# Optimization experiments

Hardware: AMD Instinct MI355X
Metric: run time of the kernel (lower is better)

## Reference

```python
import jax, jax.numpy as jnp
import numpy as np

B, L, HID, H = 2, 384, 512, 8
D = HID // H  # head_dim = 64


def setup_inputs() -> dict:
    key = jax.random.key(0)
    ks = jax.random.split(key, 16)
    s = 0.02
    return {
        "query": jax.random.normal(ks[0], (B, L, HID), jnp.float32),
        "key_": jax.random.normal(ks[1], (B, L, HID), jnp.float32),
        "value": jax.random.normal(ks[2], (B, L, HID), jnp.float32),
        "mask": jnp.ones((B, 1, 1, L), jnp.int32),
        # fc_q/k/v/o: nn.Linear(hid_dim, hid_dim)
        "Wq": jax.random.normal(ks[3], (HID, HID), jnp.float32) * s,
        "bq": jnp.zeros((HID,), jnp.float32),
        "Wk": jax.random.normal(ks[4], (HID, HID), jnp.float32) * s,
        "bk": jnp.zeros((HID,), jnp.float32),
        "Wv": jax.random.normal(ks[5], (HID, HID), jnp.float32) * s,
        "bv": jnp.zeros((HID,), jnp.float32),
        "Wo": jax.random.normal(ks[6], (HID, HID), jnp.float32) * s,
        "bo": jnp.zeros((HID,), jnp.float32),
        # additive-attention score MLP: W1, W2: Linear(D, D); v: Linear(D, 1)
        "W1": jax.random.normal(ks[7], (D, D), jnp.float32) * s,
        "b1": jnp.zeros((D,), jnp.float32),
        "W2": jax.random.normal(ks[8], (D, D), jnp.float32) * s,
        "b2": jnp.zeros((D,), jnp.float32),
        "vw": jax.random.normal(ks[9], (1, D), jnp.float32) * s,
        "vb": jnp.zeros((1,), jnp.float32),
    }


def reference(query, key_, value, mask, Wq, bq, Wk, bk, Wv, bv, Wo, bo,
              W1, b1, W2, b2, vw, vb):
    b = query.shape[0]
    # projections (torch Linear: x @ W.T + b)
    Q = query @ Wq.T + bq
    K = key_ @ Wk.T + bk
    V = value @ Wv.T + bv
    # [b, h, l, d]
    def split_heads(x):
        return x.reshape(b, -1, H, D).transpose(0, 2, 1, 3)
    Q, K, V = split_heads(Q), split_heads(K), split_heads(V)
    # additive (Bahdanau-style) score: v^T tanh(W1 q + W2 k)
    tQ = Q @ W1.T + b1            # [b, h, lq, d]
    tK = K @ W2.T + b2            # [b, h, lk, d]
    e = jnp.tanh(tQ[:, :, :, None, :] + tK[:, :, None, :, :])  # [b,h,lq,lk,d]
    energy = jnp.einsum('bhqkd,d->bhqk', e, vw[0]) + vb[0]      # [b,h,lq,lk]
    energy = jnp.where(mask == 0, jnp.float32(-1e10), energy)
    attention = jax.nn.softmax(energy, axis=-1)
    x = jnp.einsum('bhqk,bhkd->bhqd', attention, V)  # dropout p=0 (eval)
    x = x.transpose(0, 2, 1, 3).reshape(b, -1, HID)
    x = x @ Wo.T + bo
    return x, attention
```

## Files before the change

### kernel.cpp

```cpp
#include <hip/hip_runtime.h>

#define BATCH 2
#define LSEQ 384
#define NHID 512
#define NH 8
#define DH 64
#define BH (BATCH*NH)
#define MROWS (BATCH*LSEQ)
#define XELEMS ((size_t)MROWS * NHID)
#define TQ 4
#define QTILES (LSEQ/TQ)

typedef unsigned short ushort_t;

__device__ __forceinline__ float bf2f(ushort_t u) {
    unsigned int v = ((unsigned int)u) << 16;
    return __uint_as_float(v);
}
__device__ __forceinline__ ushort_t f2bf(float f) {
    unsigned int u = __float_as_uint(f);
    unsigned int lsb = (u >> 16) & 1u;
    u += 0x7fffu + lsb;
    return (ushort_t)(u >> 16);
}
__device__ __forceinline__ float ld1(const void* p, size_t i, int f) {
    return f ? ((const float*)p)[i] : bf2f(((const ushort_t*)p)[i]);
}
__device__ __forceinline__ float4 ld4(const void* p, size_t i, int f) {
    if (f) return ((const float4*)p)[i >> 2];
    ushort4 u = ((const ushort4*)p)[i >> 2];
    return make_float4(bf2f(u.x), bf2f(u.y), bf2f(u.z), bf2f(u.w));
}
__device__ __forceinline__ int block_detect(const unsigned int* q, int* cnt) {
    int t = threadIdx.x;
    if (t == 0) *cnt = 0;
    __syncthreads();
    int n = blockDim.x < 256 ? blockDim.x : 256;
    if (t < n) {
        unsigned int elo = (q[t] >> 7) & 0xFFu;
        if (elo >= 100u && elo <= 150u) atomicAdd(cnt, 1);
    }
    __syncthreads();
    return (*cnt * 2 > n) ? 0 : 1;
}

#define OFF_P     16
#define PSTRIDE   393216
#define OFF_BQE   2359312
#define OFF_BKE   2359824
#define OFF_ETQ   2360336
#define OFF_ETKT  2753552
#define OFF_VH    3146768
#define OFF_XH    3539984

#define MICRO_FMA(a, b)                                                  \
    acc[0][0] = fmaf(a.x, b.x, acc[0][0]); acc[0][1] = fmaf(a.x, b.y, acc[0][1]); \
    acc[0][2] = fmaf(a.x, b.z, acc[0][2]); acc[0][3] = fmaf(a.x, b.w, acc[0][3]); \
    acc[1][0] = fmaf(a.y, b.x, acc[1][0]); acc[1][1] = fmaf(a.y, b.y, acc[1][1]); \
    acc[1][2] = fmaf(a.y, b.z, acc[1][2]); acc[1][3] = fmaf(a.y, b.w, acc[1][3]); \
    acc[2][0] = fmaf(a.z, b.x, acc[2][0]); acc[2][1] = fmaf(a.z, b.y, acc[2][1]); \
    acc[2][2] = fmaf(a.z, b.z, acc[2][2]); acc[2][3] = fmaf(a.z, b.w, acc[2][3]); \
    acc[3][0] = fmaf(a.w, b.x, acc[3][0]); acc[3][1] = fmaf(a.w, b.y, acc[3][1]); \
    acc[3][2] = fmaf(a.w, b.z, acc[3][2]); acc[3][3] = fmaf(a.w, b.w, acc[3][3])

#define FMA4(dst, p, v)  dst.x = fmaf(p, v.x, dst.x); dst.y = fmaf(p, v.y, dst.y); \
                         dst.z = fmaf(p, v.z, dst.z); dst.w = fmaf(p, v.w, dst.w)

__global__ __launch_bounds__(128) void gemm_qkv(
    const void* qp, const void* kp, const void* vp,
    const void* Wqp, const void* Wkp, const void* Wvp,
    const void* W1p, const void* W2p,
    const void* bqp, const void* bkp, const void* b1p, const void* b2p,
    float* __restrict__ ws)
{
    __shared__ int s_cnt;
    __shared__ __align__(16) float smem[6656];
    const int f = block_detect((const unsigned int*)qp, &s_cnt);

    const int z = blockIdx.z;
    const int mode = z >> 1, ks = z & 1;
    const int kbase = ks * 256;
    const void* A = (mode == 0) ? qp : (mode == 1) ? kp : vp;
    const void* W = (mode == 0) ? Wqp : (mode == 1) ? Wkp : Wvp;
    float* P = ws + OFF_P + (size_t)z * PSTRIDE;

    float* As = smem;
    float* Bs = smem + 1152;

    const int row0 = blockIdx.y * 32;
    const int col0 = blockIdx.x * 64;
    const int tid = threadIdx.x;

    const int alr = tid >> 2, alc = tid & 3;
    const int blr = tid >> 1, blc = tid & 1;
    const int tm = tid >> 4, tn = tid & 15;

    const size_t abase = (size_t)(row0 + alr) * 512;
    const size_t bbase = (size_t)(col0 + blr) * 512;

    float4 a0, a1, b0, b1, b2, b3;
    a0 = ld4(A, abase + kbase + alc * 4, f);
    a1 = ld4(A, abase + kbase + (alc + 4) * 4, f);
    b0 = ld4(W, bbase + kbase + (blc + 0) * 4, f);
    b1 = ld4(W, bbase + kbase + (blc + 2) * 4, f);
    b2 = ld4(W, bbase + kbase + (blc + 4) * 4, f);
    b3 = ld4(W, bbase + kbase + (blc + 6) * 4, f);

    float acc[4][4];
    #pragma unroll
    for (int i = 0; i < 4; i++)
        #pragma unroll
        for (int j = 0; j < 4; j++) acc[i][j] = 0.f;

    for (int k0 = kbase; k0 < kbase + 256; k0 += 32) {
        __syncthreads();
        As[(alc * 4 + 0) * 36 + alr] = a0.x; As[(alc * 4 + 1) * 36 + alr] = a0.y;
        As[(alc * 4 + 2) * 36 + alr] = a0.z; As[(alc * 4 + 3) * 36 + alr] = a0.w;
        As[((alc + 4) * 4 + 0) * 36 + alr] = a1.x; As[((alc + 4) * 4 + 1) * 36 + alr] = a1.y;
        As[((alc + 4) * 4 + 2) * 36 + alr] = a1.z; As[((alc + 4) * 4 + 3) * 36 + alr] = a1.w;
        Bs[((blc + 0) * 4 + 0) * 68 + blr] = b0.x; Bs[((blc + 0) * 4 + 1) * 68 + blr] = b0.y;
        Bs[((blc + 0) * 4 + 2) * 68 + blr] = b0.z; Bs[((blc + 0) * 4 + 3) * 68 + blr] = b0.w;
        Bs[((blc + 2) * 4 + 0) * 68 + blr] = b1.x; Bs[((blc + 2) * 4 + 1) * 68 + blr] = b1.y;
        Bs[((blc + 2) * 4 + 2) * 68 + blr] = b1.z; Bs[((blc + 2) * 4 + 3) * 68 + blr] = b1.w;
        Bs[((blc + 4) * 4 + 0) * 68 + blr] = b2.x; Bs[((blc + 4) * 4 + 1) * 68 + blr] = b2.y;
        Bs[((blc + 4) * 4 + 2) * 68 + blr] = b2.z; Bs[((blc + 4) * 4 + 3) * 68 + blr] = b2.w;
        Bs[((blc + 6) * 4 + 0) * 68 + blr] = b3.x; Bs[((blc + 6) * 4 + 1) * 68 + blr] = b3.y;
        Bs[((blc + 6) * 4 + 2) * 68 + blr] = b3.z; Bs[((blc + 6) * 4 + 3) * 68 + blr] = b3.w;
        __syncthreads();
        int k1 = k0 + 32;
        if (k1 < kbase + 256) {
            a0 = ld4(A, abase + k1 + alc * 4, f);
            a1 = ld4(A, abase + k1 + (alc + 4) * 4, f);
            b0 = ld4(W, bbase + k1 + (blc + 0) * 4, f);
            b1 = ld4(W, bbase + k1 + (blc + 2) * 4, f);
            b2 = ld4(W, bbase + k1 + (blc + 4) * 4, f);
            b3 = ld4(W, bbase + k1 + (blc + 6) * 4, f);
        }
        #pragma unroll
        for (int kk = 0; kk < 32; kk++) {
            float4 a = *reinterpret_cast<const float4*>(&As[kk * 36 + tm * 4]);
            float4 b = *reinterpret_cast<const float4*>(&Bs[kk * 68 + tn * 4]);
            MICRO_FMA(a, b);
        }
    }

    if (mode == 2) {
        #pragma unroll
        for (int i = 0; i < 4; i++) {
            int m = row0 + tm * 4 + i;
            float4 o4 = make_float4(acc[i][0], acc[i][1], acc[i][2], acc[i][3]);
            *reinterpret_cast<float4*>(&P[(size_t)m * 512 + col0 + tn * 4]) = o4;
        }
    } else {
        const void* W1x = mode ? W2p : W1p;
        float* Qs  = smem;
        float* W1s = smem + 2304;
        __syncthreads();
        #pragma unroll
        for (int i = 0; i < 4; i++)
            #pragma unroll
            for (int j = 0; j < 4; j++)
                Qs[(tn * 4 + j) * 36 + tm * 4 + i] = acc[i][j];
        {
            int od = tid >> 1;
            #pragma unroll
            for (int c = 0; c < 8; c++) {
                int j = (tid & 1) * 32 + c * 4;
                float4 w = ld4(W1x, (size_t)od * 64 + j, f);
                W1s[(j + 0) * 68 + od] = w.x; W1s[(j + 1) * 68 + od] = w.y;
                W1s[(j + 2) * 68 + od] = w.z; W1s[(j + 3) * 68 + od] = w.w;
            }
        }
        __syncthreads();
        float facc[4][4];
        #pragma unroll
        for (int i = 0; i < 4; i++)
            #pragma unroll
            for (int j = 0; j < 4; j++) facc[i][j] = 0.f;
        {
            float acc[4][4];
            #pragma unroll
            for (int i = 0; i < 4; i++)
                #pragma unroll
                for (int j = 0; j < 4; j++) acc[i][j] = 0.f;
            #pragma unroll 8
            for (int kk = 0; kk < 64; kk++) {
                float4 a = *reinterpret_cast<const float4*>(&Qs[kk * 36 + tm * 4]);
                float4 b = *reinterpret_cast<const float4*>(&W1s[kk * 68 + tn * 4]);
                MICRO_FMA(a, b);
            }
            #pragma unroll
            for (int i = 0; i < 4; i++)
                #pragma unroll
                for (int j = 0; j < 4; j++) facc[i][j] = acc[i][j];
        }
        #pragma unroll
        for (int i = 0; i < 4; i++) {
            int m = row0 + tm * 4 + i;
            float4 o4 = make_float4(facc[i][0], facc[i][1], facc[i][2], facc[i][3]);
            *reinterpret_cast<float4*>(&P[(size_t)m * 512 + col0 + tn * 4]) = o4;
        }
        if (blockIdx.y == 0 && ks == 0 && tid < 64) {
            int o = col0 + tid, od = o & 63, h = o >> 6;
            const void* b1x = mode ? b2p : b1p;
            const void* bx  = mode ? bkp : bqp;
            float s = ld1(b1x, od, f);
            for (int j = 0; j < 64; j++)
                s = fmaf(ld1(W1x, (size_t)od * 64 + j, f), ld1(bx, h * 64 + j, f), s);
            ws[(mode ? OFF_BKE : OFF_BQE) + o] = s;
        }
    }
}

__global__ __launch_bounds__(256) void finalize(
    const void* qp, const void* bvp,
    const float* __restrict__ ws_in, float* __restrict__ ws)
{
    __shared__ int s_cnt;
    __shared__ __align__(16) float T[64 * 68];
    const int f = block_detect((const unsigned int*)qp, &s_cnt);
    const int blk = blockIdx.x;
    const int tid = threadIdx.x;

    if (blk < 384 || blk >= 480) {
        const int isV = (blk >= 480);
        const float* P0 = ws_in + OFF_P + (size_t)(isV ? 4 : 0) * PSTRIDE;
        const float* P1 = P0 + PSTRIDE;
        float* Out = ws + (isV ? OFF_VH : OFF_ETQ);
        int gid = (isV ? blk - 480 : blk) * 256 + tid;
        int m = gid >> 7;
        int o4 = (gid & 127) * 4;
        float4 p0 = *reinterpret_cast<const float4*>(P0 + (size_t)m * 512 + o4);
        float4 p1 = *reinterpret_cast<const float4*>(P1 + (size_t)m * 512 + o4);
        float4 bb;
        if (isV) bb = ld4(bvp, o4, f);
        else     bb = *reinterpret_cast<const float4*>(ws_in + OFF_BQE + o4);
        float4 r;
        if (isV) {
            r.x = p0.x + p1.x + bb.x; r.y = p0.y + p1.y + bb.y;
            r.z = p0.z + p1.z + bb.z; r.w = p0.w + p1.w + bb.w;
        } else {
            r.x = __expf(2.f * (p0.x + p1.x + bb.x));
            r.y = __expf(2.f * (p0.y + p1.y + bb.y));
            r.z = __expf(2.f * (p0.z + p1.z + bb.z));
            r.w = __expf(2.f * (p0.w + p1.w + bb.w));
        }
        int b = m / LSEQ, l = m % LSEQ, h = o4 >> 6, d = o4 & 63;
        *reinterpret_cast<float4*>(&Out[(size_t)((b * NH + h) * LSEQ + l) * 64 + d]) = r;
    } else {
        int blk2 = blk - 384;
        int bh = blk2 / 6, l0 = (blk2 % 6) * 64;
        int b = bh >> 3, h = bh & 7;
        const float* P0 = ws_in + OFF_P + (size_t)2 * PSTRIDE;
        const float* P1 = P0 + PSTRIDE;
        #pragma unroll
        for (int it = 0; it < 4; it++) {
            int li = (tid >> 4) + it * 16;
            int d4 = (tid & 15) * 4;
            size_t src = (size_t)(b * LSEQ + l0 + li) * 512 + h * 64 + d4;
            float4 p0 = *reinterpret_cast<const float4*>(P0 + src);
            float4 p1 = *reinterpret_cast<const float4*>(P1 + src);
            const float4 bb = *reinterpret_cast<const float4*>(ws_in + OFF_BKE + h * 64 + d4);
            T[(d4 + 0) * 68 + li] = __expf(2.f * (p0.x + p1.x + bb.x));
            T[(d4 + 1) * 68 + li] = __expf(2.f * (p0.y + p1.y + bb.y));
            T[(d4 + 2) * 68 + li] = __expf(2.f * (p0.z + p1.z + bb.z));
            T[(d4 + 3) * 68 + li] = __expf(2.f * (p0.w + p1.w + bb.w));
        }
        __syncthreads();
        float* Out = ws + OFF_ETKT;
        #pragma unroll
        for (int it = 0; it < 4; it++) {
            int d = (tid >> 4) + it * 16;
            int l4 = (tid & 15) * 4;
            float4 v = *reinterpret_cast<const float4*>(&T[d * 68 + l4]);
            *reinterpret_cast<float4*>(&Out[(size_t)(bh * 64 + d) * LSEQ + l0 + l4]) = v;
        }
    }
}

__global__ __launch_bounds__(384, 6) void attn_kernel(
    const void* qp, const void* vwp, const void* vbp,
    const float* __restrict__ ws_in, float* __restrict__ ws,
    const int* __restrict__ mask, void* __restrict__ dout)
{
    __shared__ int s_cnt;
    const int f = block_detect((const unsigned int*)qp, &s_cnt);

    const float* Etq = ws_in + OFF_ETQ;
    const float* Etk = ws_in + OFF_ETKT;
    const float* Vh  = ws_in + OFF_VH;
    float* Xh = ws + OFF_XH;

    const int bid = blockIdx.x;
    const int qt = bid % QTILES;
    const int bh = bid / QTILES;
    const int q0 = qt * TQ;
    const int b  = bh >> 3;
    const int h  = bh & 7;
    const int t  = threadIdx.x;
    const int wave = t >> 6;

    __shared__ __align__(16) float etqT[64][TQ];
    __shared__ float iws[64];
    __shared__ float ps[TQ][LSEQ];
    __shared__ float red[6][TQ][16][4];
    __shared__ float rmax[TQ][6];
    __shared__ float rsum[TQ][6];
    __shared__ float s_vb;

    if (t < 256) {
        int d = t & 63, qi = t >> 6;
        float vwv = ld1(vwp, d, f);
        float iw = __builtin_amdgcn_rcpf(vwv);
        etqT[d][qi] = Etq[(size_t)(bh * LSEQ + q0 + qi) * 64 + d] * iw;
        if (qi == 0) {
            iws[d] = iw;
            float v = vwv;
            #pragma unroll
            for (int off = 32; off > 0; off >>= 1) v += __shfl_xor(v, off, 64);
            if (d == 0) s_vb = ld1(vbp, 0, f) + v;
        }
    }
    const int mok = mask[b * LSEQ + t];
    __syncthreads();
    const float vbSum = s_vb;

    float e2[TQ] = {0.f, 0.f, 0.f, 0.f};
    const float* ekp = Etk + (size_t)bh * 64 * LSEQ + t;
    #pragma unroll 4
    for (int d = 0; d < 64; d++) {
        float ekv = ekp[(size_t)d * LSEQ];
        float4 eq = *reinterpret_cast<const float4*>(&etqT[d][0]);
        float iw = iws[d];
        e2[0] += __builtin_amdgcn_rcpf(fmaf(eq.x, ekv, iw));
        e2[1] += __builtin_amdgcn_rcpf(fmaf(eq.y, ekv, iw));
        e2[2] += __builtin_amdgcn_rcpf(fmaf(eq.z, ekv, iw));
        e2[3] += __builtin_amdgcn_rcpf(fmaf(eq.w, ekv, iw));
    }
    float en[TQ];
    #pragma unroll
    for (int qi = 0; qi < TQ; qi++) {
        en[qi] = fmaf(-2.0f, e2[qi], vbSum);
        if (mok == 0) en[qi] = -1e10f;
    }

    #pragma unroll
    for (int qi = 0; qi < TQ; qi++) {
        float m = en[qi];
        #pragma unroll
        for (int off = 32; off > 0; off >>= 1) m = fmaxf(m, __shfl_xor(m, off, 64));
        if ((t & 63) == 0) rmax[qi][wave] = m;
    }
    __syncthreads();
    float p[TQ];
    #pragma unroll
    for (int qi = 0; qi < TQ; qi++) {
        float gm = fmaxf(fmaxf(fmaxf(rmax[qi][0], rmax[qi][1]),
                               fmaxf(rmax[qi][2], rmax[qi][3])),
                         fmaxf(rmax[qi][4], rmax[qi][5]));
        p[qi] = __expf(en[qi] - gm);
        float s = p[qi];
        #pragma unroll
        for (int off = 32; off > 0; off >>= 1) s += __shfl_xor(s, off, 64);
        if ((t & 63) == 0) rsum[qi][wave] = s;
    }
    __syncthreads();
    #pragma unroll
    for (int qi = 0; qi < TQ; qi++) {
        float gs = rsum[qi][0] + rsum[qi][1] + rsum[qi][2] +
                   rsum[qi][3] + rsum[qi][4] + rsum[qi][5];
        p[qi] *= 1.0f / gs;
        ps[qi][t] = p[qi];
        size_t aidx = XELEMS + (size_t)(bh * LSEQ + q0 + qi) * LSEQ + t;
        if (f) ((float*)dout)[aidx] = p[qi];
        else   ((ushort_t*)dout)[aidx] = f2bf(p[qi]);
    }
    __syncthreads();

    const int dq = t & 15;
    const int ksub = t >> 4;
    const float* vb4 = Vh + (size_t)bh * LSEQ * 64 + dq * 4;
    float4 acc[TQ];
    #pragma unroll
    for (int qi = 0; qi < TQ; qi++) acc[qi] = make_float4(0.f, 0.f, 0.f, 0.f);
    for (int kk = ksub; kk < LSEQ; kk += 24) {
        float4 v4 = *reinterpret_cast<const float4*>(vb4 + (size_t)kk * 64);
        #pragma unroll
        for (int qi = 0; qi < TQ; qi++) {
            float pq = ps[qi][kk];
            FMA4(acc[qi], pq, v4);
        }
    }
    #pragma unroll
    for (int qi = 0; qi < TQ; qi++) {
        #pragma unroll
        for (int off = 16; off <= 32; off <<= 1) {
            acc[qi].x += __shfl_xor(acc[qi].x, off, 64);
            acc[qi].y += __shfl_xor(acc[qi].y, off, 64);
            acc[qi].z += __shfl_xor(acc[qi].z, off, 64);
            acc[qi].w += __shfl_xor(acc[qi].w, off, 64);
        }
    }
    if ((t & 63) < 16) {
        #pragma unroll
        for (int qi = 0; qi < TQ; qi++) {
            red[wave][qi][dq][0] = acc[qi].x;
            red[wave][qi][dq][1] = acc[qi].y;
            red[wave][qi][dq][2] = acc[qi].z;
            red[wave][qi][dq][3] = acc[qi].w;
        }
    }
    __syncthreads();
    if (t < 256) {
        int qi = t >> 6, d = t & 63;
        float sx = 0.f;
        #pragma unroll
        for (int w = 0; w < 6; w++) sx += red[w][qi][d >> 2][d & 3];
        Xh[((size_t)(b * LSEQ + q0 + qi) * NH + h) * 64 + d] = sx;
    }
}

__global__ __launch_bounds__(128) void gemm_out(
    const void* qp, const void* Wop, const void* bop,
    const float* __restrict__ ws_in, void* __restrict__ dout)
{
    __shared__ int s_cnt;
    __shared__ __align__(16) float As[32][36];
    __shared__ __align__(16) float Bs[32][68];
    const int f = block_detect((const unsigned int*)qp, &s_cnt);

    const float* Xh = ws_in + OFF_XH;
    const int row0 = blockIdx.y * 32;
    const int col0 = blockIdx.x * 64;
    const int tid = threadIdx.x;

    const int alr = tid >> 2, alc = tid & 3;
    const int blr = tid >> 1, blc = tid & 1;
    const int tm = tid >> 4, tn = tid & 15;

    const float* Ab = Xh + (size_t)(row0 + alr) * 512;
    const size_t bbase = (size_t)(col0 + blr) * 512;

    float4 a0, a1, b0, b1, b2, b3;
    a0 = *reinterpret_cast<const float4*>(Ab + alc * 4);
    a1 = *reinterpret_cast<const float4*>(Ab + (alc + 4) * 4);
    b0 = ld4(Wop, bbase + (blc + 0) * 4, f);
    b1 = ld4(Wop, bbase + (blc + 2) * 4, f);
    b2 = ld4(Wop, bbase + (blc + 4) * 4, f);
    b3 = ld4(Wop, bbase + (blc + 6) * 4, f);

    float acc[4][4];
    #pragma unroll
    for (int i = 0; i < 4; i++)
        #pragma unroll
        for (int j = 0; j < 4; j++) acc[i][j] = 0.f;

    for (int k0 = 0; k0 < 512; k0 += 32) {
        __syncthreads();
        As[alc * 4 + 0][alr] = a0.x; As[alc * 4 + 1][alr] = a0.y;
        As[alc * 4 + 2][alr] = a0.z; As[alc * 4 + 3][alr] = a0.w;
        As[(alc + 4) * 4 + 0][alr] = a1.x; As[(alc + 4) * 4 + 1][alr] = a1.y;
        As[(alc + 4) * 4 + 2][alr] = a1.z; As[(alc + 4) * 4 + 3][alr] = a1.w;
        Bs[(blc + 0) * 4 + 0][blr] = b0.x; Bs[(blc + 0) * 4 + 1][blr] = b0.y;
        Bs[(blc + 0) * 4 + 2][blr] = b0.z; Bs[(blc + 0) * 4 + 3][blr] = b0.w;
        Bs[(blc + 2) * 4 + 0][blr] = b1.x; Bs[(blc + 2) * 4 + 1][blr] = b1.y;
        Bs[(blc + 2) * 4 + 2][blr] = b1.z; Bs[(blc + 2) * 4 + 3][blr] = b1.w;
        Bs[(blc + 4) * 4 + 0][blr] = b2.x; Bs[(blc + 4) * 4 + 1][blr] = b2.y;
        Bs[(blc + 4) * 4 + 2][blr] = b2.z; Bs[(blc + 4) * 4 + 3][blr] = b2.w;
        Bs[(blc + 6) * 4 + 0][blr] = b3.x; Bs[(blc + 6) * 4 + 1][blr] = b3.y;
        Bs[(blc + 6) * 4 + 2][blr] = b3.z; Bs[(blc + 6) * 4 + 3][blr] = b3.w;
        __syncthreads();
        int k1 = k0 + 32;
        if (k1 < 512) {
            a0 = *reinterpret_cast<const float4*>(Ab + k1 + alc * 4);
            a1 = *reinterpret_cast<const float4*>(Ab + k1 + (alc + 4) * 4);
            b0 = ld4(Wop, bbase + k1 + (blc + 0) * 4, f);
            b1 = ld4(Wop, bbase + k1 + (blc + 2) * 4, f);
            b2 = ld4(Wop, bbase + k1 + (blc + 4) * 4, f);
            b3 = ld4(Wop, bbase + k1 + (blc + 6) * 4, f);
        }
        #pragma unroll
        for (int kk = 0; kk < 32; kk++) {
            float4 a = *reinterpret_cast<const float4*>(&As[kk][tm * 4]);
            float4 b = *reinterpret_cast<const float4*>(&Bs[kk][tn * 4]);
            MICRO_FMA(a, b);
        }
    }

    #pragma unroll
    for (int i = 0; i < 4; i++) {
        int m = row0 + tm * 4 + i;
        #pragma unroll
        for (int j = 0; j < 4; j++) {
            int n = col0 + tn * 4 + j;
            float c = acc[i][j] + ld1(bop, n, f);
            size_t idx = (size_t)m * 512 + n;
            if (f) ((float*)dout)[idx] = c;
            else   ((ushort_t*)dout)[idx] = f2bf(c);
        }
    }
}

extern "C" void kernel_launch(void* const* d_in, const int* in_sizes, int n_in,
                              void* d_out, int out_size, void* d_ws, size_t ws_size,
                              hipStream_t stream)
{
    const void* qp = d_in[0];
    const void* kp = d_in[1];
    const void* vp = d_in[2];
    const int* mask = (const int*)d_in[3];
    const void* Wqp = d_in[4];  const void* bqp = d_in[5];
    const void* Wkp = d_in[6];  const void* bkp = d_in[7];
    const void* Wvp = d_in[8];  const void* bvp = d_in[9];
    const void* Wop = d_in[10]; const void* bop = d_in[11];
    const void* W1p = d_in[12]; const void* b1p = d_in[13];
    const void* W2p = d_in[14]; const void* b2p = d_in[15];
    const void* vwp = d_in[16]; const void* vbp = d_in[17];

    float* ws = (float*)d_ws;

    gemm_qkv<<<dim3(8, 24, 6), 128, 0, stream>>>(qp, kp, vp, Wqp, Wkp, Wvp,
                                                 W1p, W2p, bqp, bkp, b1p, b2p, ws);
    finalize<<<864, 256, 0, stream>>>(qp, bvp, ws, ws);
    attn_kernel<<<BH * QTILES, 384, 0, stream>>>(qp, vwp, vbp, ws, ws, mask, d_out);
    gemm_out<<<dim3(8, 24, 1), 128, 0, stream>>>(qp, Wop, bop, ws, d_out);
}
```

Baseline: 188.5 us.

## Split-K the output projection and restructure the additive-score inner loop

The output projection GEMM is split four ways along K, writing partial tiles to workspace, and a new reduction kernel sums the partials, adds the bias and converts to the output type. This raises block count from 192 to 768 to fill more compute units, at the cost of an extra launch and partial-buffer traffic. The attention kernel drops the shared-memory staging of scaled query terms and instead reads Etq rows and vw directly in the loop, using a 1.0 offset with an fma by vw rather than pre-dividing by vw. A redundant accumulator copy in the QKV GEMM epilogue is also removed.

```diff
diff --git a/kernel.cpp b/kernel.cpp
--- a/kernel.cpp
+++ b/kernel.cpp
@@ -172,11 +172,6 @@
             }
         }
         __syncthreads();
-        float facc[4][4];
-        #pragma unroll
-        for (int i = 0; i < 4; i++)
-            #pragma unroll
-            for (int j = 0; j < 4; j++) facc[i][j] = 0.f;
         {
             float acc[4][4];
             #pragma unroll
@@ -190,15 +185,11 @@
                 MICRO_FMA(a, b);
             }
             #pragma unroll
-            for (int i = 0; i < 4; i++)
-                #pragma unroll
-                for (int j = 0; j < 4; j++) facc[i][j] = acc[i][j];
-        }
-        #pragma unroll
-        for (int i = 0; i < 4; i++) {
-            int m = row0 + tm * 4 + i;
-            float4 o4 = make_float4(facc[i][0], facc[i][1], facc[i][2], facc[i][3]);
-            *reinterpret_cast<float4*>(&P[(size_t)m * 512 + col0 + tn * 4]) = o4;
+            for (int i = 0; i < 4; i++) {
+                int m = row0 + tm * 4 + i;
+                float4 o4 = make_float4(acc[i][0], acc[i][1], acc[i][2], acc[i][3]);
+                *reinterpret_cast<float4*>(&P[(size_t)m * 512 + col0 + tn * 4]) = o4;
+            }
         }
         if (blockIdx.y == 0 && ks == 0 && tid < 64) {
             int o = col0 + tid, od = o & 63, h = o >> 6;
@@ -300,42 +291,37 @@
     const int t  = threadIdx.x;
     const int wave = t >> 6;
 
-    __shared__ __align__(16) float etqT[64][TQ];
-    __shared__ float iws[64];
     __shared__ float ps[TQ][LSEQ];
     __shared__ float red[6][TQ][16][4];
     __shared__ float rmax[TQ][6];
     __shared__ float rsum[TQ][6];
     __shared__ float s_vb;
 
-    if (t < 256) {
-        int d = t & 63, qi = t >> 6;
-        float vwv = ld1(vwp, d, f);
-        float iw = __builtin_amdgcn_rcpf(vwv);
-        etqT[d][qi] = Etq[(size_t)(bh * LSEQ + q0 + qi) * 64 + d] * iw;
-        if (qi == 0) {
-            iws[d] = iw;
-            float v = vwv;
-            #pragma unroll
-            for (int off = 32; off > 0; off >>= 1) v += __shfl_xor(v, off, 64);
-            if (d == 0) s_vb = ld1(vbp, 0, f) + v;
-        }
+    if (t < 64) {
+        float v = ld1(vwp, t, f);
+        #pragma unroll
+        for (int off = 32; off > 0; off >>= 1) v += __shfl_xor(v, off, 64);
+        if (t == 0) s_vb = ld1(vbp, 0, f) + v;
     }
     const int mok = mask[b * LSEQ + t];
     __syncthreads();
     const float vbSum = s_vb;
 
+    const float* eqr0 = Etq + (size_t)(bh * LSEQ + q0) * 64;
+    const float* eqr1 = eqr0 + 64;
+    const float* eqr2 = eqr0 + 128;
+    const float* eqr3 = eqr0 + 192;
+    const float* ekp  = Etk + (size_t)bh * 64 * LSEQ + t;
+
     float e2[TQ] = {0.f, 0.f, 0.f, 0.f};
-    const float* ekp = Etk + (size_t)bh * 64 * LSEQ + t;
     #pragma unroll 4
     for (int d = 0; d < 64; d++) {
         float ekv = ekp[(size_t)d * LSEQ];
-        float4 eq = *reinterpret_cast<const float4*>(&etqT[d][0]);
-        float iw = iws[d];
-        e2[0] += __builtin_amdgcn_rcpf(fmaf(eq.x, ekv, iw));
-        e2[1] += __builtin_amdgcn_rcpf(fmaf(eq.y, ekv, iw));
-        e2[2] += __builtin_amdgcn_rcpf(fmaf(eq.z, ekv, iw));
-        e2[3] += __builtin_amdgcn_rcpf(fmaf(eq.w, ekv, iw));
+        float w = ld1(vwp, d, f);
+        e2[0] = fmaf(w, __builtin_amdgcn_rcpf(fmaf(eqr0[d], ekv, 1.0f)), e2[0]);
+        e2[1] = fmaf(w, __builtin_amdgcn_rcpf(fmaf(eqr1[d], ekv, 1.0f)), e2[1]);
+        e2[2] = fmaf(w, __builtin_amdgcn_rcpf(fmaf(eqr2[d], ekv, 1.0f)), e2[2]);
+        e2[3] = fmaf(w, __builtin_amdgcn_rcpf(fmaf(eqr3[d], ekv, 1.0f)), e2[3]);
     }
     float en[TQ];
     #pragma unroll
@@ -421,8 +407,8 @@
 }
 
 __global__ __launch_bounds__(128) void gemm_out(
-    const void* qp, const void* Wop, const void* bop,
-    const float* __restrict__ ws_in, void* __restrict__ dout)
+    const void* qp, const void* Wop,
+    const float* __restrict__ ws_in, float* __restrict__ ws)
 {
     __shared__ int s_cnt;
     __shared__ __align__(16) float As[32][36];
@@ -430,6 +416,10 @@
     const int f = block_detect((const unsigned int*)qp, &s_cnt);
 
     const float* Xh = ws_in + OFF_XH;
+    const int ks = blockIdx.z;
+    const int kbase = ks * 128;
+    float* P = ws + OFF_P + (size_t)ks * PSTRIDE;
+
     const int row0 = blockIdx.y * 32;
     const int col0 = blockIdx.x * 64;
     const int tid = threadIdx.x;
@@ -438,8 +428,8 @@
     const int blr = tid >> 1, blc = tid & 1;
     const int tm = tid >> 4, tn = tid & 15;
 
-    const float* Ab = Xh + (size_t)(row0 + alr) * 512;
-    const size_t bbase = (size_t)(col0 + blr) * 512;
+    const float* Ab = Xh + (size_t)(row0 + alr) * 512 + kbase;
+    const size_t bbase = (size_t)(col0 + blr) * 512 + kbase;
 
     float4 a0, a1, b0, b1, b2, b3;
     a0 = *reinterpret_cast<const float4*>(Ab + alc * 4);
@@ -455,7 +445,7 @@
         #pragma unroll
         for (int j = 0; j < 4; j++) acc[i][j] = 0.f;
 
-    for (int k0 = 0; k0 < 512; k0 += 32) {
+    for (int k0 = 0; k0 < 128; k0 += 32) {
         __syncthreads();
         As[alc * 4 + 0][alr] = a0.x; As[alc * 4 + 1][alr] = a0.y;
         As[alc * 4 + 2][alr] = a0.z; As[alc * 4 + 3][alr] = a0.w;
@@ -471,7 +461,7 @@
         Bs[(blc + 6) * 4 + 2][blr] = b3.z; Bs[(blc + 6) * 4 + 3][blr] = b3.w;
         __syncthreads();
         int k1 = k0 + 32;
-        if (k1 < 512) {
+        if (k1 < 128) {
             a0 = *reinterpret_cast<const float4*>(Ab + k1 + alc * 4);
             a1 = *reinterpret_cast<const float4*>(Ab + k1 + (alc + 4) * 4);
             b0 = ld4(Wop, bbase + k1 + (blc + 0) * 4, f);
@@ -490,14 +480,37 @@
     #pragma unroll
     for (int i = 0; i < 4; i++) {
         int m = row0 + tm * 4 + i;
-        #pragma unroll
-        for (int j = 0; j < 4; j++) {
-            int n = col0 + tn * 4 + j;
-            float c = acc[i][j] + ld1(bop, n, f);
-            size_t idx = (size_t)m * 512 + n;
-            if (f) ((float*)dout)[idx] = c;
-            else   ((ushort_t*)dout)[idx] = f2bf(c);
-        }
+        float4 o4 = make_float4(acc[i][0], acc[i][1], acc[i][2], acc[i][3]);
+        *reinterpret_cast<float4*>(&P[(size_t)m * 512 + col0 + tn * 4]) = o4;
+    }
+}
+
+__global__ __launch_bounds__(256) void out_reduce(
+    const void* qp, const void* bop,
+    const float* __restrict__ ws_in, void* __restrict__ dout)
+{
+    __shared__ int s_cnt;
+    const int f = block_detect((const unsigned int*)qp, &s_cnt);
+    int gid = blockIdx.x * 256 + threadIdx.x;
+    size_t idx = (size_t)gid * 4;
+    int o4 = (int)(idx & 511);
+    const float* P = ws_in + OFF_P;
+    float4 s0 = *reinterpret_cast<const float4*>(P + idx);
+    float4 s1 = *reinterpret_cast<const float4*>(P + PSTRIDE + idx);
+    float4 s2 = *reinterpret_cast<const float4*>(P + 2 * (size_t)PSTRIDE + idx);
+    float4 s3 = *reinterpret_cast<const float4*>(P + 3 * (size_t)PSTRIDE + idx);
+    float4 bb = ld4(bop, o4, f);
+    float4 r;
+    r.x = (s0.x + s1.x) + (s2.x + s3.x) + bb.x;
+    r.y = (s0.y + s1.y) + (s2.y + s3.y) + bb.y;
+    r.z = (s0.z + s1.z) + (s2.z + s3.z) + bb.z;
+    r.w = (s0.w + s1.w) + (s2.w + s3.w) + bb.w;
+    if (f) {
+        *reinterpret_cast<float4*>((float*)dout + idx) = r;
+    } else {
+        ushort4 u;
+        u.x = f2bf(r.x); u.y = f2bf(r.y); u.z = f2bf(r.z); u.w = f2bf(r.w);
+        *reinterpret_cast<ushort4*>((ushort_t*)dout + idx) = u;
     }
 }
 
@@ -523,5 +536,6 @@
                                                  W1p, W2p, bqp, bkp, b1p, b2p, ws);
     finalize<<<864, 256, 0, stream>>>(qp, bvp, ws, ws);
     attn_kernel<<<BH * QTILES, 384, 0, stream>>>(qp, vwp, vbp, ws, ws, mask, d_out);
-    gemm_out<<<dim3(8, 24, 1), 128, 0, stream>>>(qp, Wop, bop, ws, d_out);
-}
+    gemm_out<<<dim3(8, 24, 4), 128, 0, stream>>>(qp, Wop, ws, ws);
+    out_reduce<<<384, 256, 0, stream>>>(qp, bop, ws, d_out);
+}
```

After: 183.1 us. -2.8%, faster.
